# Optimization experiments

Measured on AMD Instinct MI355X. Metric: run time of the kernel, lower is better.

The kernel has to match this reference:

```python
import jax, jax.numpy as jnp
import numpy as np

A, B, M, H, MAX_NB, N_MOLS = 100000, 200000, 20000, 256, 10, 2000
ATOM_FDIM, BOND_FDIM, DEPTH = 35, 5, 3


def setup_inputs() -> dict:
    key = jax.random.key(0)
    ks = jax.random.split(key, 10)
    fatoms = jax.random.normal(ks[0], (A, ATOM_FDIM), dtype=jnp.float32)
    fbonds = jax.random.normal(ks[1], (B, ATOM_FDIM + BOND_FDIM), dtype=jnp.float32)
    agraph = jax.random.randint(ks[2], (A, MAX_NB), 0, M + B)
    bgraph = jax.random.randint(ks[3], (B, MAX_NB), 0, M + B)
    tree_message = jax.random.normal(ks[4], (M, H), dtype=jnp.float32)
    tree_message = tree_message.at[0].set(0.0)  # all_mess[0] is the zero pad vector
    atom_scope = jnp.sort(jax.random.randint(ks[5], (A,), 0, N_MOLS))
    s = 1.0 / np.sqrt(H)
    W_i = jax.random.normal(ks[6], (ATOM_FDIM + BOND_FDIM, H), dtype=jnp.float32) * s
    W_h = jax.random.normal(ks[7], (H, H), dtype=jnp.float32) * s
    W_o_w = jax.random.normal(ks[8], (ATOM_FDIM + H, H), dtype=jnp.float32) * s
    W_o_b = jax.random.normal(ks[9], (H,), dtype=jnp.float32) * s
    return {"fatoms": fatoms, "fbonds": fbonds, "agraph": agraph, "bgraph": bgraph,
            "tree_message": tree_message, "atom_scope": atom_scope,
            "W_i": W_i, "W_h": W_h, "W_o_w": W_o_w, "W_o_b": W_o_b}


def reference(fatoms, fbonds, agraph, bgraph, tree_message, atom_scope, W_i, W_h, W_o_w, W_o_b):
    binput = fbonds @ W_i                       # [B, H]
    graph_message = jax.nn.relu(binput)
    for _ in range(DEPTH - 1):
        message = jnp.concatenate([tree_message, graph_message], axis=0)  # [M+B, H]
        nei = message[bgraph].sum(axis=1)       # gather [B, MAX_NB, H] -> sum -> [B, H]
        graph_message = jax.nn.relu(binput + nei @ W_h)
    message = jnp.concatenate([tree_message, graph_message], axis=0)
    nei = message[agraph].sum(axis=1)           # [A, H]
    ainput = jnp.concatenate([fatoms, nei], axis=1)  # [A, ATOM_FDIM + H]
    atom_hiddens = jax.nn.relu(ainput @ W_o_w + W_o_b)
    # scope-based segment-mean pooling over atoms of each molecule
    sums = jax.ops.segment_sum(atom_hiddens, atom_scope, num_segments=N_MOLS)
    counts = jax.ops.segment_sum(jnp.ones((atom_hiddens.shape[0],), atom_hiddens.dtype),
                                 atom_scope, num_segments=N_MOLS)
    return sums / jnp.maximum(counts, 1.0)[:, None]
```

## Files before the change

kernel.cpp:

```cpp
#include <hip/hip_runtime.h>
#include <cstdint>
#include <cstddef>

#define A_N 100000
#define B_N 200000
#define M_N 20000
#define POOL_N 220000
#define HD 256
#define MAX_NB 10
#define N_MOLS 2000
#define ATOM_FDIM 35
#define FB_DIM 40

typedef unsigned short u16;
typedef __attribute__((ext_vector_type(8))) short bf16x8;
typedef __attribute__((ext_vector_type(4))) float f32x4;

__device__ u16 g_msg0[(size_t)B_N * HD];
__device__ u16 g_msg1[(size_t)B_N * HD];
__device__ u16 g_tmsgh[(size_t)M_N * HD];
__device__ u16 g_P[(size_t)POOL_N * HD];
__device__ u16 g_Q[(size_t)POOL_N * HD];
__device__ u16 g_binH[(size_t)B_N * HD];
__device__ float g_F[(size_t)A_N * HD];
__device__ u16 g_pWh_hi[65536], g_pWh_lo[65536];
__device__ u16 g_pWo_hi[65536], g_pWo_lo[65536];
__device__ float g_counts[N_MOLS];

__device__ __forceinline__ u16 f2b(float f)
{
    union { float f; unsigned u; } x; x.f = f;
    const unsigned r = x.u + 0x7FFFu + ((x.u >> 16) & 1u);
    return (u16)(r >> 16);
}
__device__ __forceinline__ float b2f(u16 h) { return __uint_as_float((unsigned)h << 16); }
__device__ __forceinline__ float blo(unsigned u) { return __uint_as_float(u << 16); }
__device__ __forceinline__ float bhi(unsigned u) { return __uint_as_float(u & 0xffff0000u); }

__global__ __launch_bounds__(256)
void k_zero_out(float* __restrict__ p, int n)
{
    const int i = blockIdx.x * 256 + threadIdx.x;
    if (i < n) p[i] = 0.f;
}

__global__ __launch_bounds__(256)
void k_zero_counts()
{
    const int i = blockIdx.x * 256 + threadIdx.x;
    if (i < N_MOLS) g_counts[i] = 0.f;
}

__global__ __launch_bounds__(256)
void k_cvt(const float* __restrict__ tmsg)
{
    const int i = (blockIdx.x * 256 + threadIdx.x) * 4;
    if (i < M_N * HD) {
        const float4 v = *(const float4*)(tmsg + i);
        ushort4 o;
        o.x = f2b(v.x); o.y = f2b(v.y); o.z = f2b(v.z); o.w = f2b(v.w);
        *(ushort4*)(g_tmsgh + i) = o;
    }
}

__global__ __launch_bounds__(256)
void k_packW(const float* __restrict__ Wh, const float* __restrict__ Wo)
{
    const int id = blockIdx.x * 256 + threadIdx.x;
    if (id >= 8192) return;
    const int l = id & 63;
    const int t = (id >> 6) & 15;
    const int c = id >> 10;
    const int n = t * 16 + (l & 15);
    const int kb = c * 32 + ((l >> 4) << 3);
    const size_t base = (size_t)id * 8;
    #pragma unroll
    for (int j = 0; j < 8; ++j) {
        const int k = kb + j;
        const float wh = Wh[(size_t)k * HD + n];
        const u16 hh = f2b(wh);
        g_pWh_hi[base + j] = hh;
        g_pWh_lo[base + j] = f2b(wh - b2f(hh));
        const float wo = Wo[(size_t)(35 + k) * HD + n];
        const u16 oh = f2b(wo);
        g_pWo_hi[base + j] = oh;
        g_pWo_lo[base + j] = f2b(wo - b2f(oh));
    }
}

__global__ __launch_bounds__(256, 2)
void k_in(const float* __restrict__ fbonds, const float* __restrict__ Wi)
{
    const int lane = threadIdx.x & 63;
    const int wid  = (blockIdx.x * 256 + threadIdx.x) >> 6;
    const int nw   = (gridDim.x * 256) >> 6;

    float4 w[FB_DIM];
    #pragma unroll
    for (int k = 0; k < FB_DIM; ++k)
        w[k] = *(const float4*)&Wi[(size_t)k * HD + lane * 4];

    #pragma unroll 1
    for (int row = wid; row < B_N; row += nw) {
        const float* fr = fbonds + (size_t)row * FB_DIM;
        float ax = 0.f, ay = 0.f, az = 0.f, aw = 0.f;
        #pragma unroll
        for (int q = 0; q < FB_DIM / 4; ++q) {
            const float4 fv = *(const float4*)(fr + q * 4);
            ax += fv.x * w[q*4+0].x; ay += fv.x * w[q*4+0].y;
            az += fv.x * w[q*4+0].z; aw += fv.x * w[q*4+0].w;
            ax += fv.y * w[q*4+1].x; ay += fv.y * w[q*4+1].y;
            az += fv.y * w[q*4+1].z; aw += fv.y * w[q*4+1].w;
            ax += fv.z * w[q*4+2].x; ay += fv.z * w[q*4+2].y;
            az += fv.z * w[q*4+2].z; aw += fv.z * w[q*4+2].w;
            ax += fv.w * w[q*4+3].x; ay += fv.w * w[q*4+3].y;
            az += fv.w * w[q*4+3].z; aw += fv.w * w[q*4+3].w;
        }
        const size_t base = (size_t)row * HD + lane * 4;
        ushort4 bi;
        bi.x = f2b(ax); bi.y = f2b(ay); bi.z = f2b(az); bi.w = f2b(aw);
        *(ushort4*)(g_binH + base) = bi;
        ushort4 o;
        o.x = f2b(fmaxf(ax, 0.f)); o.y = f2b(fmaxf(ay, 0.f));
        o.z = f2b(fmaxf(az, 0.f)); o.w = f2b(fmaxf(aw, 0.f));
        *(ushort4*)(g_msg0 + base) = o;
    }
}

__global__ __launch_bounds__(256, 2)
void k_gemmMF(int sel, int rowStart, int rowEnd)
{
    const u16* msrc = (sel == 1) ? g_msg1 : g_msg0;
    const u16* pHi  = (sel == 2) ? g_pWo_hi : g_pWh_hi;
    const u16* pLo  = (sel == 2) ? g_pWo_lo : g_pWh_lo;
    u16* dst        = (sel == 2) ? g_Q : g_P;

    const int tid  = threadIdx.x;
    const int lane = tid & 63;
    const int wv   = tid >> 6;
    const int l15  = lane & 15;
    const int quad = lane >> 4;
    const int tOff = (wv & 1) * 8;

    int rowIdeal[4];
    const u16* srow[4];
    #pragma unroll
    for (int rg = 0; rg < 4; ++rg) {
        const int ri = rowStart + blockIdx.x * 128 + (wv >> 1) * 64 + rg * 16 + l15;
        rowIdeal[rg] = ri;
        const int r = (ri < rowEnd) ? ri : (rowEnd - 1);
        srow[rg] = (r < M_N) ? (g_tmsgh + (size_t)r * HD)
                             : (msrc + (size_t)(r - M_N) * HD);
    }

    f32x4 acc[4][8];
    #pragma unroll
    for (int rg = 0; rg < 4; ++rg)
        #pragma unroll
        for (int t = 0; t < 8; ++t)
            acc[rg][t] = (f32x4){0.f, 0.f, 0.f, 0.f};

    #pragma unroll 1
    for (int c = 0; c < 8; ++c) {
        bf16x8 b[4];
        #pragma unroll
        for (int rg = 0; rg < 4; ++rg)
            b[rg] = *(const bf16x8*)(srow[rg] + c * 32 + quad * 8);
        const u16* ph = pHi + ((size_t)(c * 16 + tOff) * 64 + lane) * 8;
        const u16* pl = pLo + ((size_t)(c * 16 + tOff) * 64 + lane) * 8;
        #pragma unroll
        for (int t = 0; t < 8; ++t) {
            const bf16x8 ah = *(const bf16x8*)(ph + (size_t)t * 512);
            #pragma unroll
            for (int rg = 0; rg < 4; ++rg)
                acc[rg][t] = __builtin_amdgcn_mfma_f32_16x16x32_bf16(ah, b[rg], acc[rg][t], 0, 0, 0);
            const bf16x8 al = *(const bf16x8*)(pl + (size_t)t * 512);
            #pragma unroll
            for (int rg = 0; rg < 4; ++rg)
                acc[rg][t] = __builtin_amdgcn_mfma_f32_16x16x32_bf16(al, b[rg], acc[rg][t], 0, 0, 0);
        }
    }

    #pragma unroll
    for (int rg = 0; rg < 4; ++rg) {
        if (rowIdeal[rg] < rowEnd) {
            u16* drow = dst + (size_t)rowIdeal[rg] * HD + tOff * 16 + quad * 4;
            #pragma unroll
            for (int t = 0; t < 8; ++t) {
                ushort4 o;
                o.x = f2b(acc[rg][t][0]); o.y = f2b(acc[rg][t][1]);
                o.z = f2b(acc[rg][t][2]); o.w = f2b(acc[rg][t][3]);
                *(ushort4*)(drow + t * 16) = o;
            }
        }
    }
}

__global__ __launch_bounds__(256)
void k_gather(const int* __restrict__ bgraph, int dstSel)
{
    u16* dst = dstSel ? g_msg1 : g_msg0;
    __shared__ int idx_s[8][MAX_NB];
    const int tid = threadIdx.x;
    const int rowBase = blockIdx.x * 8;
    if (tid < 8 * MAX_NB) {
        const int r = tid / MAX_NB;
        const int j = tid - r * MAX_NB;
        idx_s[r][j] = bgraph[(size_t)(rowBase + r) * MAX_NB + j];
    }
    __syncthreads();
    const int rl = tid >> 5;
    const int c  = (tid & 31) << 3;
    const int row = rowBase + rl;

    float s[8] = {0.f,0.f,0.f,0.f,0.f,0.f,0.f,0.f};
    #pragma unroll
    for (int j = 0; j < MAX_NB; ++j) {
        const uint4 v = *(const uint4*)(g_P + (size_t)idx_s[rl][j] * HD + c);
        s[0] += blo(v.x); s[1] += bhi(v.x);
        s[2] += blo(v.y); s[3] += bhi(v.y);
        s[4] += blo(v.z); s[5] += bhi(v.z);
        s[6] += blo(v.w); s[7] += bhi(v.w);
    }
    const uint4 bv = *(const uint4*)(g_binH + (size_t)row * HD + c);
    uint4 w;
    w.x = ((unsigned)f2b(fmaxf(s[0] + blo(bv.x), 0.f)))
        | ((unsigned)f2b(fmaxf(s[1] + bhi(bv.x), 0.f)) << 16);
    w.y = ((unsigned)f2b(fmaxf(s[2] + blo(bv.y), 0.f)))
        | ((unsigned)f2b(fmaxf(s[3] + bhi(bv.y), 0.f)) << 16);
    w.z = ((unsigned)f2b(fmaxf(s[4] + blo(bv.z), 0.f)))
        | ((unsigned)f2b(fmaxf(s[5] + bhi(bv.z), 0.f)) << 16);
    w.w = ((unsigned)f2b(fmaxf(s[6] + blo(bv.w), 0.f)))
        | ((unsigned)f2b(fmaxf(s[7] + bhi(bv.w), 0.f)) << 16);
    *(uint4*)(dst + (size_t)row * HD + c) = w;
}

__global__ __launch_bounds__(256, 2)
void k_F(const float* __restrict__ fatoms, const float* __restrict__ Wo,
         const float* __restrict__ bias)
{
    const int lane = threadIdx.x & 63;
    const int wid  = (blockIdx.x * 256 + threadIdx.x) >> 6;
    const int nw   = (gridDim.x * 256) >> 6;

    float4 w[ATOM_FDIM];
    #pragma unroll
    for (int k = 0; k < ATOM_FDIM; ++k)
        w[k] = *(const float4*)&Wo[(size_t)k * HD + lane * 4];
    const float4 b4 = *(const float4*)&bias[lane * 4];

    #pragma unroll 1
    for (int row = wid; row < A_N; row += nw) {
        const float* fr = fatoms + (size_t)row * ATOM_FDIM;
        float ax = b4.x, ay = b4.y, az = b4.z, aw = b4.w;
        #pragma unroll
        for (int k = 0; k < ATOM_FDIM; ++k) {
            const float f = fr[k];
            ax += f * w[k].x; ay += f * w[k].y;
            az += f * w[k].z; aw += f * w[k].w;
        }
        float4 o; o.x = ax; o.y = ay; o.z = az; o.w = aw;
        *(float4*)(g_F + (size_t)row * HD + lane * 4) = o;
    }
}

__global__ __launch_bounds__(256)
void k_gatherA(const int* __restrict__ agraph, const int* __restrict__ scope,
               float* __restrict__ out)
{
    __shared__ int idx_s[64 * MAX_NB];
    __shared__ int sc_s[64];
    const int tid = threadIdx.x;
    const int rb = blockIdx.x * 64;
    for (int i = tid; i < 64 * MAX_NB; i += 256) {
        const int a = rb + i / MAX_NB;
        idx_s[i] = (a < A_N) ? agraph[(size_t)a * MAX_NB + (i % MAX_NB)] : 0;
    }
    if (tid < 64) sc_s[tid] = (rb + tid < A_N) ? scope[rb + tid] : -1;
    __syncthreads();

    const int grp = tid >> 5;
    const int c = (tid & 31) * 8;
    float s[8] = {0.f,0.f,0.f,0.f,0.f,0.f,0.f,0.f};
    int prev = -1;
    #pragma unroll 1
    for (int i = 0; i < 8; ++i) {
        const int al = grp * 8 + i;
        const int a = rb + al;
        if (a < A_N) {
            const int m = sc_s[al];
            if (m != prev) {
                if (prev >= 0) {
                    float* dst = out + (size_t)prev * HD + c;
                    #pragma unroll
                    for (int q = 0; q < 8; ++q) atomicAdd(dst + q, s[q]);
                    #pragma unroll
                    for (int q = 0; q < 8; ++q) s[q] = 0.f;
                }
                prev = m;
            }
            float g0=0.f,g1=0.f,g2=0.f,g3=0.f,g4=0.f,g5=0.f,g6=0.f,g7=0.f;
            #pragma unroll
            for (int j = 0; j < MAX_NB; ++j) {
                const uint4 v = *(const uint4*)(g_Q + (size_t)idx_s[al * MAX_NB + j] * HD + c);
                g0 += blo(v.x); g1 += bhi(v.x);
                g2 += blo(v.y); g3 += bhi(v.y);
                g4 += blo(v.z); g5 += bhi(v.z);
                g6 += blo(v.w); g7 += bhi(v.w);
            }
            const float4 f0 = *(const float4*)(g_F + (size_t)a * HD + c);
            const float4 f1 = *(const float4*)(g_F + (size_t)a * HD + c + 4);
            s[0] += fmaxf(g0 + f0.x, 0.f); s[1] += fmaxf(g1 + f0.y, 0.f);
            s[2] += fmaxf(g2 + f0.z, 0.f); s[3] += fmaxf(g3 + f0.w, 0.f);
            s[4] += fmaxf(g4 + f1.x, 0.f); s[5] += fmaxf(g5 + f1.y, 0.f);
            s[6] += fmaxf(g6 + f1.z, 0.f); s[7] += fmaxf(g7 + f1.w, 0.f);
        }
    }
    if (prev >= 0) {
        float* dst = out + (size_t)prev * HD + c;
        #pragma unroll
        for (int q = 0; q < 8; ++q) atomicAdd(dst + q, s[q]);
    }
}

__global__ __launch_bounds__(256)
void k_counts(const int* __restrict__ scope)
{
    const int a = blockIdx.x * 256 + threadIdx.x;
    if (a < A_N) atomicAdd(&g_counts[scope[a]], 1.0f);
}

__global__ __launch_bounds__(256)
void k_div(float* __restrict__ out)
{
    const int idx = blockIdx.x * 256 + threadIdx.x;
    out[idx] = out[idx] / fmaxf(g_counts[idx >> 8], 1.0f);
}

extern "C" void kernel_launch(void* const* d_in, const int* in_sizes, int n_in,
                              void* d_out, int out_size, void* d_ws, size_t ws_size,
                              hipStream_t stream)
{
    const float* fatoms = (const float*)d_in[0];
    const float* fbonds = (const float*)d_in[1];
    const int*   agraph = (const int*)d_in[2];
    const int*   bgraph = (const int*)d_in[3];
    const float* tmsg   = (const float*)d_in[4];
    const int*   scope  = (const int*)d_in[5];
    const float* W_i    = (const float*)d_in[6];
    const float* W_h    = (const float*)d_in[7];
    const float* W_o    = (const float*)d_in[8];
    const float* W_ob   = (const float*)d_in[9];
    float* out = (float*)d_out;

    (void)d_ws; (void)ws_size;

    k_zero_out<<<(N_MOLS * HD + 255) / 256, 256, 0, stream>>>(out, N_MOLS * HD);
    k_zero_counts<<<(N_MOLS + 255) / 256, 256, 0, stream>>>();
    k_cvt<<<(M_N * HD / 4 + 255) / 256, 256, 0, stream>>>(tmsg);
    k_packW<<<32, 256, 0, stream>>>(W_h, W_o);

    k_in<<<512, 256, 0, stream>>>(fbonds, W_i);

    k_gemmMF<<<(POOL_N + 127) / 128, 256, 0, stream>>>(0, 0, POOL_N);
    k_gather<<<B_N / 8, 256, 0, stream>>>(bgraph, 1);
    k_gemmMF<<<(B_N + 127) / 128, 256, 0, stream>>>(1, M_N, POOL_N);
    k_gather<<<B_N / 8, 256, 0, stream>>>(bgraph, 0);

    k_gemmMF<<<(POOL_N + 127) / 128, 256, 0, stream>>>(2, 0, POOL_N);
    k_F<<<512, 256, 0, stream>>>(fatoms, W_o, W_ob);
    k_counts<<<(A_N + 255) / 256, 256, 0, stream>>>(scope);
    k_gatherA<<<(A_N + 63) / 64, 256, 0, stream>>>(agraph, scope, out);
    k_div<<<(N_MOLS * HD) / 256, 256, 0, stream>>>(out);
}
```

Before: 1.310 ms.

## Fuse setup kernels, store F in bf16, prefetch GEMM operands, chunk gathers

Merges the zero, convert, weight-pack and count kernels into one setup launch, and computes per-molecule counts by binary search over the sorted scope instead of atomics. Stores the atom-feature projection F as bf16, which halves its write and read traffic at some cost in precision. The GEMM loop software-prefetches the next K-chunk of B operands. The gathers hoist the binput load ahead of the neighbor loop and are split into four sequential launches over row ranges, which adds launch overhead for a possible gain in cache locality.

Result: no change. 1.288 ms (-1.6%).

```diff
diff --git a/kernel.cpp b/kernel.cpp
--- a/kernel.cpp
+++ b/kernel.cpp
@@ -22,7 +22,7 @@
 __device__ u16 g_P[(size_t)POOL_N * HD];
 __device__ u16 g_Q[(size_t)POOL_N * HD];
 __device__ u16 g_binH[(size_t)B_N * HD];
-__device__ float g_F[(size_t)A_N * HD];
+__device__ u16 g_Fh[(size_t)A_N * HD];
 __device__ u16 g_pWh_hi[65536], g_pWh_lo[65536];
 __device__ u16 g_pWo_hi[65536], g_pWo_lo[65536];
 __device__ float g_counts[N_MOLS];
@@ -37,54 +37,57 @@
 __device__ __forceinline__ float blo(unsigned u) { return __uint_as_float(u << 16); }
 __device__ __forceinline__ float bhi(unsigned u) { return __uint_as_float(u & 0xffff0000u); }
 
+__device__ __forceinline__ int lbound(const int* __restrict__ s, int n, int v)
+{
+    int l = 0, r = n;
+    while (l < r) { const int mid = (l + r) >> 1; if (s[mid] < v) l = mid + 1; else r = mid; }
+    return l;
+}
+
 __global__ __launch_bounds__(256)
-void k_zero_out(float* __restrict__ p, int n)
-{
-    const int i = blockIdx.x * 256 + threadIdx.x;
-    if (i < n) p[i] = 0.f;
-}
-
-__global__ __launch_bounds__(256)
-void k_zero_counts()
-{
-    const int i = blockIdx.x * 256 + threadIdx.x;
-    if (i < N_MOLS) g_counts[i] = 0.f;
-}
-
-__global__ __launch_bounds__(256)
-void k_cvt(const float* __restrict__ tmsg)
-{
-    const int i = (blockIdx.x * 256 + threadIdx.x) * 4;
-    if (i < M_N * HD) {
-        const float4 v = *(const float4*)(tmsg + i);
-        ushort4 o;
-        o.x = f2b(v.x); o.y = f2b(v.y); o.z = f2b(v.z); o.w = f2b(v.w);
-        *(ushort4*)(g_tmsgh + i) = o;
-    }
-}
-
-__global__ __launch_bounds__(256)
-void k_packW(const float* __restrict__ Wh, const float* __restrict__ Wo)
-{
-    const int id = blockIdx.x * 256 + threadIdx.x;
-    if (id >= 8192) return;
-    const int l = id & 63;
-    const int t = (id >> 6) & 15;
-    const int c = id >> 10;
-    const int n = t * 16 + (l & 15);
-    const int kb = c * 32 + ((l >> 4) << 3);
-    const size_t base = (size_t)id * 8;
-    #pragma unroll
-    for (int j = 0; j < 8; ++j) {
-        const int k = kb + j;
-        const float wh = Wh[(size_t)k * HD + n];
-        const u16 hh = f2b(wh);
-        g_pWh_hi[base + j] = hh;
-        g_pWh_lo[base + j] = f2b(wh - b2f(hh));
-        const float wo = Wo[(size_t)(35 + k) * HD + n];
-        const u16 oh = f2b(wo);
-        g_pWo_hi[base + j] = oh;
-        g_pWo_lo[base + j] = f2b(wo - b2f(oh));
+void k_setup(float* __restrict__ out, const float* __restrict__ tmsg,
+             const float* __restrict__ Wh, const float* __restrict__ Wo,
+             const int* __restrict__ scope)
+{
+    const int bid = blockIdx.x;
+    const int tid = threadIdx.x;
+    if (bid < 2000) {
+        out[bid * 256 + tid] = 0.f;
+    } else if (bid < 7000) {
+        const int i = ((bid - 2000) * 256 + tid) * 4;
+        if (i < M_N * HD) {
+            const float4 v = *(const float4*)(tmsg + i);
+            ushort4 o;
+            o.x = f2b(v.x); o.y = f2b(v.y); o.z = f2b(v.z); o.w = f2b(v.w);
+            *(ushort4*)(g_tmsgh + i) = o;
+        }
+    } else if (bid < 7032) {
+        const int id = (bid - 7000) * 256 + tid;
+        const int l = id & 63;
+        const int t = (id >> 6) & 15;
+        const int c = id >> 10;
+        const int n = t * 16 + (l & 15);
+        const int kb = c * 32 + ((l >> 4) << 3);
+        const size_t base = (size_t)id * 8;
+        #pragma unroll
+        for (int j = 0; j < 8; ++j) {
+            const int k = kb + j;
+            const float wh = Wh[(size_t)k * HD + n];
+            const u16 hh = f2b(wh);
+            g_pWh_hi[base + j] = hh;
+            g_pWh_lo[base + j] = f2b(wh - b2f(hh));
+            const float wo = Wo[(size_t)(35 + k) * HD + n];
+            const u16 oh = f2b(wo);
+            g_pWo_hi[base + j] = oh;
+            g_pWo_lo[base + j] = f2b(wo - b2f(oh));
+        }
+    } else {
+        const int m = (bid - 7032) * 256 + tid;
+        if (m < N_MOLS) {
+            const int lo = lbound(scope, A_N, m);
+            const int hi = lbound(scope, A_N, m + 1);
+            g_counts[m] = (float)(hi - lo);
+        }
     }
 }
 
@@ -160,25 +163,34 @@
         for (int t = 0; t < 8; ++t)
             acc[rg][t] = (f32x4){0.f, 0.f, 0.f, 0.f};
 
+    bf16x8 b0 = *(const bf16x8*)(srow[0] + quad * 8);
+    bf16x8 b1 = *(const bf16x8*)(srow[1] + quad * 8);
+    bf16x8 b2 = *(const bf16x8*)(srow[2] + quad * 8);
+    bf16x8 b3 = *(const bf16x8*)(srow[3] + quad * 8);
+
     #pragma unroll 1
     for (int c = 0; c < 8; ++c) {
-        bf16x8 b[4];
-        #pragma unroll
-        for (int rg = 0; rg < 4; ++rg)
-            b[rg] = *(const bf16x8*)(srow[rg] + c * 32 + quad * 8);
+        const int cn = (c + 1) & 7;
+        const bf16x8 n0 = *(const bf16x8*)(srow[0] + cn * 32 + quad * 8);
+        const bf16x8 n1 = *(const bf16x8*)(srow[1] + cn * 32 + quad * 8);
+        const bf16x8 n2 = *(const bf16x8*)(srow[2] + cn * 32 + quad * 8);
+        const bf16x8 n3 = *(const bf16x8*)(srow[3] + cn * 32 + quad * 8);
         const u16* ph = pHi + ((size_t)(c * 16 + tOff) * 64 + lane) * 8;
         const u16* pl = pLo + ((size_t)(c * 16 + tOff) * 64 + lane) * 8;
         #pragma unroll
         for (int t = 0; t < 8; ++t) {
             const bf16x8 ah = *(const bf16x8*)(ph + (size_t)t * 512);
-            #pragma unroll
-            for (int rg = 0; rg < 4; ++rg)
-                acc[rg][t] = __builtin_amdgcn_mfma_f32_16x16x32_bf16(ah, b[rg], acc[rg][t], 0, 0, 0);
+            acc[0][t] = __builtin_amdgcn_mfma_f32_16x16x32_bf16(ah, b0, acc[0][t], 0, 0, 0);
+            acc[1][t] = __builtin_amdgcn_mfma_f32_16x16x32_bf16(ah, b1, acc[1][t], 0, 0, 0);
+            acc[2][t] = __builtin_amdgcn_mfma_f32_16x16x32_bf16(ah, b2, acc[2][t], 0, 0, 0);
+            acc[3][t] = __builtin_amdgcn_mfma_f32_16x16x32_bf16(ah, b3, acc[3][t], 0, 0, 0);
             const bf16x8 al = *(const bf16x8*)(pl + (size_t)t * 512);
-            #pragma unroll
-            for (int rg = 0; rg < 4; ++rg)
-                acc[rg][t] = __builtin_amdgcn_mfma_f32_16x16x32_bf16(al, b[rg], acc[rg][t], 0, 0, 0);
-        }
+            acc[0][t] = __builtin_amdgcn_mfma_f32_16x16x32_bf16(al, b0, acc[0][t], 0, 0, 0);
+            acc[1][t] = __builtin_amdgcn_mfma_f32_16x16x32_bf16(al, b1, acc[1][t], 0, 0, 0);
+            acc[2][t] = __builtin_amdgcn_mfma_f32_16x16x32_bf16(al, b2, acc[2][t], 0, 0, 0);
+            acc[3][t] = __builtin_amdgcn_mfma_f32_16x16x32_bf16(al, b3, acc[3][t], 0, 0, 0);
+        }
+        b0 = n0; b1 = n1; b2 = n2; b3 = n3;
     }
 
     #pragma unroll
@@ -197,12 +209,12 @@
 }
 
 __global__ __launch_bounds__(256)
-void k_gather(const int* __restrict__ bgraph, int dstSel)
+void k_gather(const int* __restrict__ bgraph, int dstSel, int rowOff)
 {
     u16* dst = dstSel ? g_msg1 : g_msg0;
     __shared__ int idx_s[8][MAX_NB];
     const int tid = threadIdx.x;
-    const int rowBase = blockIdx.x * 8;
+    const int rowBase = rowOff + blockIdx.x * 8;
     if (tid < 8 * MAX_NB) {
         const int r = tid / MAX_NB;
         const int j = tid - r * MAX_NB;
@@ -213,6 +225,7 @@
     const int c  = (tid & 31) << 3;
     const int row = rowBase + rl;
 
+    const uint4 bv = *(const uint4*)(g_binH + (size_t)row * HD + c);
     float s[8] = {0.f,0.f,0.f,0.f,0.f,0.f,0.f,0.f};
     #pragma unroll
     for (int j = 0; j < MAX_NB; ++j) {
@@ -222,7 +235,6 @@
         s[4] += blo(v.z); s[5] += bhi(v.z);
         s[6] += blo(v.w); s[7] += bhi(v.w);
     }
-    const uint4 bv = *(const uint4*)(g_binH + (size_t)row * HD + c);
     uint4 w;
     w.x = ((unsigned)f2b(fmaxf(s[0] + blo(bv.x), 0.f)))
         | ((unsigned)f2b(fmaxf(s[1] + bhi(bv.x), 0.f)) << 16);
@@ -259,8 +271,9 @@
             ax += f * w[k].x; ay += f * w[k].y;
             az += f * w[k].z; aw += f * w[k].w;
         }
-        float4 o; o.x = ax; o.y = ay; o.z = az; o.w = aw;
-        *(float4*)(g_F + (size_t)row * HD + lane * 4) = o;
+        ushort4 o;
+        o.x = f2b(ax); o.y = f2b(ay); o.z = f2b(az); o.w = f2b(aw);
+        *(ushort4*)(g_Fh + (size_t)row * HD + lane * 4) = o;
     }
 }
 
@@ -299,6 +312,7 @@
                 }
                 prev = m;
             }
+            const uint4 fv = *(const uint4*)(g_Fh + (size_t)a * HD + c);
             float g0=0.f,g1=0.f,g2=0.f,g3=0.f,g4=0.f,g5=0.f,g6=0.f,g7=0.f;
             #pragma unroll
             for (int j = 0; j < MAX_NB; ++j) {
@@ -308,12 +322,10 @@
                 g4 += blo(v.z); g5 += bhi(v.z);
                 g6 += blo(v.w); g7 += bhi(v.w);
             }
-            const float4 f0 = *(const float4*)(g_F + (size_t)a * HD + c);
-            const float4 f1 = *(const float4*)(g_F + (size_t)a * HD + c + 4);
-            s[0] += fmaxf(g0 + f0.x, 0.f); s[1] += fmaxf(g1 + f0.y, 0.f);
-            s[2] += fmaxf(g2 + f0.z, 0.f); s[3] += fmaxf(g3 + f0.w, 0.f);
-            s[4] += fmaxf(g4 + f1.x, 0.f); s[5] += fmaxf(g5 + f1.y, 0.f);
-            s[6] += fmaxf(g6 + f1.z, 0.f); s[7] += fmaxf(g7 + f1.w, 0.f);
+            s[0] += fmaxf(g0 + blo(fv.x), 0.f); s[1] += fmaxf(g1 + bhi(fv.x), 0.f);
+            s[2] += fmaxf(g2 + blo(fv.y), 0.f); s[3] += fmaxf(g3 + bhi(fv.y), 0.f);
+            s[4] += fmaxf(g4 + blo(fv.z), 0.f); s[5] += fmaxf(g5 + bhi(fv.z), 0.f);
+            s[6] += fmaxf(g6 + blo(fv.w), 0.f); s[7] += fmaxf(g7 + bhi(fv.w), 0.f);
         }
     }
     if (prev >= 0) {
@@ -321,13 +333,6 @@
         #pragma unroll
         for (int q = 0; q < 8; ++q) atomicAdd(dst + q, s[q]);
     }
-}
-
-__global__ __launch_bounds__(256)
-void k_counts(const int* __restrict__ scope)
-{
-    const int a = blockIdx.x * 256 + threadIdx.x;
-    if (a < A_N) atomicAdd(&g_counts[scope[a]], 1.0f);
 }
 
 __global__ __launch_bounds__(256)
@@ -355,21 +360,18 @@
 
     (void)d_ws; (void)ws_size;
 
-    k_zero_out<<<(N_MOLS * HD + 255) / 256, 256, 0, stream>>>(out, N_MOLS * HD);
-    k_zero_counts<<<(N_MOLS + 255) / 256, 256, 0, stream>>>();
-    k_cvt<<<(M_N * HD / 4 + 255) / 256, 256, 0, stream>>>(tmsg);
-    k_packW<<<32, 256, 0, stream>>>(W_h, W_o);
-
+    k_setup<<<7040, 256, 0, stream>>>(out, tmsg, W_h, W_o, scope);
     k_in<<<512, 256, 0, stream>>>(fbonds, W_i);
 
     k_gemmMF<<<(POOL_N + 127) / 128, 256, 0, stream>>>(0, 0, POOL_N);
-    k_gather<<<B_N / 8, 256, 0, stream>>>(bgraph, 1);
+    for (int ch = 0; ch < 4; ++ch)
+        k_gather<<<B_N / 32, 256, 0, stream>>>(bgraph, 1, ch * (B_N / 4));
     k_gemmMF<<<(B_N + 127) / 128, 256, 0, stream>>>(1, M_N, POOL_N);
-    k_gather<<<B_N / 8, 256, 0, stream>>>(bgraph, 0);
+    for (int ch = 0; ch < 4; ++ch)
+        k_gather<<<B_N / 32, 256, 0, stream>>>(bgraph, 0, ch * (B_N / 4));
 
     k_gemmMF<<<(POOL_N + 127) / 128, 256, 0, stream>>>(2, 0, POOL_N);
     k_F<<<512, 256, 0, stream>>>(fatoms, W_o, W_ob);
-    k_counts<<<(A_N + 255) / 256, 256, 0, stream>>>(scope);
     k_gatherA<<<(A_N + 63) / 64, 256, 0, stream>>>(agraph, scope, out);
     k_div<<<(N_MOLS * HD) / 256, 256, 0, stream>>>(out);
 }
```
